# Kernel optimization log

Measured on AMD Instinct MI355X. Metric: run time of the kernel, lower is better.

Reference implementation:

```python
import jax, jax.numpy as jnp
import numpy as np

IN_F = 135; D = 512; K = 10; DCT_N = 34; IN_N = 120; OUT_N = 24
VL = K + OUT_N          # 34, window length
VN = IN_N - K - OUT_N + 1  # 87, number of windows
NSTAGE = 2
BN_SCALE = 1.0 / np.sqrt(1.0 + 1e-5)  # eval-mode BN with default running stats (mean 0, var 1)


def get_dct_matrix(N):
    dct_m = np.eye(N)
    for k in range(N):
        for i in range(N):
            w = np.sqrt(2.0 / N)
            if k == 0:
                w = np.sqrt(1.0 / N)
            dct_m[k, i] = w * np.cos(np.pi * (i + 0.5) * k / N)
    idct_m = np.linalg.inv(dct_m)
    return dct_m, idct_m

_DCT_NP, _IDCT_NP = get_dct_matrix(VL)
DCT = jnp.asarray(_DCT_NP[:DCT_N], dtype=jnp.float32)        # [34,34] (dct_n == vl)
IDCT = jnp.asarray(_IDCT_NP[:, :DCT_N], dtype=jnp.float32)   # [34,34]

WIN_IDX = np.arange(VL)[None, :] + np.arange(VN)[:, None]    # [87,34]
PAD_IDX = np.concatenate([np.arange(IN_N - K, IN_N), np.full(OUT_N, IN_N - 1)])  # last 10 frames + last frame repeated


def conv1d(x, w):
    return jax.lax.conv_general_dilated(x, w, (1,), 'VALID',
                                        dimension_numbers=('NCH', 'OIH', 'NCH'))


def gconv(x, att, w, b):
    # GraphConvolution: att @ (x @ w) + b ; x: [b,n,f_in]
    return jnp.einsum('nm,bmf->bnf', att, x @ w) + b


def bn_eval(y, g, b):
    bs, n, f = y.shape
    v = y.reshape(bs, n * f)
    v = g * (v * BN_SCALE) + b
    return v.reshape(bs, n, f)


def setup_inputs() -> dict:
    key = jax.random.key(0)
    ks = jax.random.split(key, 20)
    s = 0.05  # small init scale so tanh/att stay in sane range
    return {
        'poses':    jax.random.normal(ks[0], (256, 144, 135), jnp.float32),
        'qw1':      jax.random.normal(ks[1], (512, 135, 6)) * s,
        'qw2':      jax.random.normal(ks[2], (512, 512, 5)) * s,
        'kw1':      jax.random.normal(ks[3], (512, 135, 6)) * s,
        'kw2':      jax.random.normal(ks[4], (512, 512, 5)) * s,
        'gc1_att':  jax.random.normal(ks[5], (135, 135)) * s,
        'gc1_w':    jax.random.normal(ks[6], (68, 512)) * s,
        'gc1_b':    jax.random.normal(ks[7], (512,)) * s,
        'bn1_g':    jnp.ones((69120,), jnp.float32),
        'bn1_b':    jnp.zeros((69120,), jnp.float32),
        'gcb_att':  jax.random.normal(ks[8], (4, 135, 135)) * s,
        'gcb_w':    jax.random.normal(ks[9], (4, 512, 512)) * s,
        'gcb_b':    jax.random.normal(ks[10], (4, 512)) * s,
        'gcb_g':    jnp.ones((4, 69120), jnp.float32),
        'gcb_beta': jnp.zeros((4, 69120), jnp.float32),
        'gc7_att':  jax.random.normal(ks[11], (135, 135)) * s,
        'gc7_w':    jax.random.normal(ks[12], (512, 68)) * s,
        'gc7_b':    jax.random.normal(ks[13], (68,)) * s,
    }


def reference(poses, qw1, qw2, kw1, kw2,
              gc1_att, gc1_w, gc1_b, bn1_g, bn1_b,
              gcb_att, gcb_w, gcb_b, gcb_g, gcb_beta,
              gc7_att, gc7_w, gc7_b):
    src = poses[:, :IN_N]                      # [b,120,135]
    bs = src.shape[0]
    src_t = jnp.transpose(src, (0, 2, 1))      # [b,135,120]
    key_in = src_t[:, :, :IN_N - OUT_N] / 1000.0   # [b,135,96]
    qry_in = src_t[:, :, -K:] / 1000.0             # [b,135,10]

    key_f = jax.nn.relu(conv1d(jax.nn.relu(conv1d(key_in, kw1)), kw2))  # [b,512,87]
    qry_f = jax.nn.relu(conv1d(jax.nn.relu(conv1d(qry_in, qw1)), qw2))  # [b,512,1]

    # non-softmax attention: matmul + eps-normalize
    score = jnp.einsum('bdq,bdk->bqk', qry_f, key_f) + 1e-15   # [b,1,87]
    att = score / jnp.sum(score, axis=2, keepdims=True)

    # overlapping windows -> DCT of each window
    windows = src[:, WIN_IDX]                                   # [b,87,34,135]
    val = jnp.einsum('kt,bvtf->bvfk', DCT, windows).reshape(bs, VN, IN_F * DCT_N)
    dct_att = jnp.einsum('bqv,bvz->bqz', att, val)[:, 0].reshape(bs, IN_F, DCT_N)

    input_gcn = src[:, PAD_IDX]                                 # [b,34,135]
    dct_in = jnp.einsum('kt,btf->bfk', DCT, input_gcn)          # [b,135,34]
    x = jnp.concatenate([dct_in, dct_att], axis=-1)             # [b,135,68]

    # GCN (eval mode: dropout = identity, BN uses running stats)
    y = jnp.tanh(bn_eval(gconv(x, gc1_att, gc1_w, gc1_b), bn1_g, bn1_b))
    for i in range(NSTAGE):
        res = y
        h = jnp.tanh(bn_eval(gconv(y, gcb_att[2 * i], gcb_w[2 * i], gcb_b[2 * i]),
                             gcb_g[2 * i], gcb_beta[2 * i]))
        h = jnp.tanh(bn_eval(gconv(h, gcb_att[2 * i + 1], gcb_w[2 * i + 1], gcb_b[2 * i + 1]),
                             gcb_g[2 * i + 1], gcb_beta[2 * i + 1]))
        y = h + res
    y = gconv(y, gc7_att, gc7_w, gc7_b) + x                     # [b,135,68]

    out = jnp.einsum('tk,bfk->btf', IDCT, y[:, :, :DCT_N])      # [b,34,135]
    preds = out[:, -OUT_N:, :]                                  # [b,24,135]
    return preds
```

## Files before the change

### kernel.cpp

```cpp
#include <hip/hip_runtime.h>
#include <math.h>

#define POSE_ROWS 144
#define NF 135
#define DD 512
#define KQ 10
#define DCTN 34
#define INN 120
#define OUTN 24
#define VN 87
#define BATCH 256
#define RP 34816
#define NODEP 136
#define BSTRIDE 69632
#define BN_SCALE 0.9999950000374997f

typedef __attribute__((ext_vector_type(8))) short short8;
typedef __attribute__((ext_vector_type(4))) float floatx4;

static __device__ __forceinline__ ushort f2bf(float f) {
    unsigned u = __builtin_bit_cast(unsigned, f);
    u = (u + 0x7FFFu + ((u >> 16) & 1u)) >> 16;
    return (ushort)u;
}
static __device__ __forceinline__ float bf2f(ushort s) {
    return __builtin_bit_cast(float, (unsigned)s << 16);
}
static __device__ __forceinline__ float tanh_fast(float x) {
    float ax = __builtin_fabsf(x);
    float e = __builtin_amdgcn_exp2f(ax * -2.885390081777927f);
    float t = (1.f - e) * __builtin_amdgcn_rcpf(1.f + e);
    return __builtin_copysignf(t, x);
}
static __device__ __forceinline__ floatx4 mf(short8 a, short8 b, floatx4 c) {
    return __builtin_amdgcn_mfma_f32_16x16x32_bf16(a, b, c, 0, 0, 0);
}

#define GLOAD_LDS(gp, lp) __builtin_amdgcn_global_load_lds( \
    (const __attribute__((address_space(1))) unsigned int*)(const void*)(gp), \
    (__attribute__((address_space(3))) unsigned int*)(void*)(lp), 16, 0, 0)

#define PB_POSES 19584
#define PB_K1B   22912
#define PB_K2B   33152
#define PB_WT1   33408
#define PB_WTB   37504
#define PB_WT7   37640
#define PB_A1    37742
#define PB_AB    38147
#define PB_A7    38249
#define PB_BN    39609
#define PB_Z     39610
#define PB_DCT   39615

__global__ __launch_bounds__(256) void prep_all(
    const float* __restrict__ poses, ushort* __restrict__ pb16,
    const float* __restrict__ kw1, const float* __restrict__ qw1,
    ushort* __restrict__ Wt1k, ushort* __restrict__ Wt1q,
    const float* __restrict__ kw2, const float* __restrict__ qw2,
    ushort* __restrict__ Wt2k, ushort* __restrict__ Wt2q,
    const float* __restrict__ gc1_w, ushort* __restrict__ WT1,
    const float* __restrict__ gcb_w, ushort* __restrict__ WTb,
    const float* __restrict__ gc7_w, ushort* __restrict__ WT7,
    const float* __restrict__ gc1_att, ushort* __restrict__ A16_1,
    const float* __restrict__ gcb_att, ushort* __restrict__ A16_B,
    const float* __restrict__ gc7_att, ushort* __restrict__ A16_7,
    const float* __restrict__ bn1_g, const float* __restrict__ bn1_b,
    const float* __restrict__ gcb_g, const float* __restrict__ gcb_beta,
    const float* __restrict__ gc1_bias, const float* __restrict__ gcb_bias,
    float* __restrict__ bnT, float* __restrict__ zpadf, float* __restrict__ dct)
{
    const int blk = blockIdx.x;
    const int tid = threadIdx.x;
    if (blk < PB_POSES) {
        int idx = blk * 256 + tid;
        int i = idx % NODEP;
        int row = (idx / NODEP) % POSE_ROWS;
        int b = idx / (NODEP * POSE_ROWS);
        float v = (i < NF) ? poses[((long long)b * POSE_ROWS + row) * NF + i] * 1e-3f : 0.f;
        pb16[idx] = f2bf(v);
    } else if (blk < PB_K1B) {
        int wi = blk - PB_POSES;
        const float* src = (wi < 1664) ? kw1 : qw1;
        ushort* dst = (wi < 1664) ? Wt1k : Wt1q;
        int idx = (wi % 1664) * 256 + tid;
        int n = idx / 832, k = idx % 832;
        int h = k / 136, i = k % 136;
        float v = (i < 135 && h < 6) ? src[((long long)n * 135 + i) * 6 + h] : 0.f;
        dst[idx] = f2bf(v);
    } else if (blk < PB_K2B) {
        int wi = blk - PB_K1B;
        const float* src = (wi < 5120) ? kw2 : qw2;
        ushort* dst = (wi < 5120) ? Wt2k : Wt2q;
        int idx = (wi % 5120) * 256 + tid;
        int n = idx / 2560, k = idx % 2560;
        int h = k / 512, i = k % 512;
        dst[idx] = f2bf(src[((long long)n * 512 + i) * 5 + h]);
    } else if (blk < PB_WT1) {
        int idx = (blk - PB_K2B) * 256 + tid;
        int n = idx / 128, k = idx % 128;
        WT1[idx] = f2bf((k < 68) ? gc1_w[(long long)k * 512 + n] : 0.f);
    } else if (blk < PB_WTB) {
        int g = (blk - PB_WT1) * 256 + tid;
        int L = g >> 18, idx = g & 262143;
        int n = idx / 512, k = idx % 512;
        WTb[g] = f2bf(gcb_w[(long long)L * 262144 + (long long)k * 512 + n]);
    } else if (blk < PB_WT7) {
        int idx = (blk - PB_WTB) * 256 + tid;
        int n = idx / 512, k = idx % 512;
        WT7[idx] = f2bf(gc7_w[(long long)k * 68 + n]);
    } else if (blk < PB_A1) {
        int idx = (blk - PB_WT7) * 256 + tid;
        if (idx < 135 * 192) {
            int r = idx / 192, c = idx % 192;
            A16_1[idx] = f2bf(c < 135 ? gc1_att[r * 135 + c] : 0.f);
        }
    } else if (blk < PB_AB) {
        int idx = (blk - PB_A1) * 256 + tid;
        int r = idx / 192, c = idx % 192;
        A16_B[idx] = f2bf(c < 135 ? gcb_att[r * 135 + c] : 0.f);
    } else if (blk < PB_A7) {
        int idx = (blk - PB_AB) * 256 + tid;
        if (idx < 135 * 192) {
            int r = idx / 192, c = idx % 192;
            A16_7[idx] = f2bf(c < 135 ? gc7_att[r * 135 + c] : 0.f);
        }
    } else if (blk < PB_BN) {
        int g = (blk - PB_A7) * 256 + tid;
        int p = g / 69632, idx = g % 69632;
        int node = idx % 136, m = idx / 136;
        const float* gs = (p == 0) ? bn1_g : (gcb_g + (p - 1) * 69120);
        const float* bs = (p == 0) ? bn1_b : (gcb_beta + (p - 1) * 69120);
        const float* bp = (p == 0) ? gc1_bias : (gcb_bias + (p - 1) * 512);
        float* gt = bnT + (long long)p * 139264;
        float gg = (node < 135) ? gs[node * 512 + m] : 0.f;
        float bb = (node < 135) ? bs[node * 512 + m] : 0.f;
        float gx = gg * BN_SCALE;
        gt[idx * 2]     = gx;
        gt[idx * 2 + 1] = gx * bp[m] + bb;
    } else if (blk < PB_Z) {
        if (tid < 128) zpadf[tid] = 0.f;
    } else {
        int idx = (blk - PB_Z) * 256 + tid;
        if (idx < DCTN * DCTN) {
            int k = idx / DCTN, i = idx % DCTN;
            double w = (k == 0) ? sqrt(1.0 / DCTN) : sqrt(2.0 / DCTN);
            dct[idx] = (float)(w * cos(3.14159265358979323846 * (i + 0.5) * k / (double)DCTN));
        }
    }
}

template<int BM, int BN>
__global__ __launch_bounds__(256) void gemm2(
    const ushort* __restrict__ A, const ushort* __restrict__ Bt,
    const ushort* __restrict__ zpad,
    int M, int N, int K,
    int mode, int CNT, int Pc,
    int rpbA, long long sAw, long long sAr, long long sAbz,
    long long sBr, long long sBbz,
    float* __restrict__ C, ushort* __restrict__ C16,
    long long sCbz, long long sCm, long long sCn,
    int do_relu, const float* __restrict__ bias, int bias_mode,
    const float* __restrict__ bnTg, const float* __restrict__ bnTb,
    int do_tanh, const ushort* __restrict__ resid16, const float* __restrict__ resid32,
    int bmaj)
{
    constexpr int SM = BM / 32, SN = BN / 32;
    constexpr int RA = BM / 32, RB = BN / 32;
    __shared__ ushort As[BM * 64];
    __shared__ ushort Bs[BN * 64];

    int mb, nb;
    if (mode == 0) { mb = blockIdx.y; nb = blockIdx.x; }
    else {
        int gx = blockIdx.x;
        int x = gx & 7, s = gx >> 3;
        if (mode == 1) { mb = s % CNT; nb = x * Pc + s / CNT; }
        else           { nb = s % CNT; mb = x * Pc + s / CNT; }
    }
    const int m0 = mb * BM, n0 = nb * BN;
    if (m0 >= M || n0 >= N) return;

    const int tid = threadIdx.x;
    const int lane = tid & 63, w = tid >> 6;
    const int bz = blockIdx.z;
    const int wm = (w >> 1) * (BM / 2), wn = (w & 1) * (BN / 2);
    const int chunk = (lane & 7) ^ ((lane >> 3) & 7);

    const ushort* pA[RA]; int stA[RA];
    #pragma unroll
    for (int j = 0; j < RA; j++) {
        int m = m0 + j * 32 + w * 8 + (lane >> 3);
        bool v = m < M;
        long long off = v ? ((long long)(m / rpbA) * sAw + (long long)(m % rpbA) * sAr
                            + (long long)bz * sAbz) : 0;
        pA[j] = v ? (A + off + chunk * 8) : (zpad + chunk * 8);
        stA[j] = v ? 64 : 0;
    }
    const ushort* pB[RB]; int stB[RB];
    #pragma unroll
    for (int j = 0; j < RB; j++) {
        int n = n0 + j * 32 + w * 8 + (lane >> 3);
        bool v = n < N;
        long long off = v ? ((long long)n * sBr + (long long)bz * sBbz) : 0;
        pB[j] = v ? (Bt + off + chunk * 8) : (zpad + chunk * 8);
        stB[j] = v ? 64 : 0;
    }

    floatx4 acc[SM][SN];
    #pragma unroll
    for (int i = 0; i < SM; i++)
        #pragma unroll
        for (int j = 0; j < SN; j++)
            acc[i][j] = (floatx4){0.f, 0.f, 0.f, 0.f};

    for (int k0 = 0; k0 < K; k0 += 64) {
        #pragma unroll
        for (int j = 0; j < RA; j++)
            GLOAD_LDS(pA[j], &As[(j * 32 + w * 8) * 64]);
        #pragma unroll
        for (int j = 0; j < RB; j++)
            GLOAD_LDS(pB[j], &Bs[(j * 32 + w * 8) * 64]);
        __syncthreads();

        #pragma unroll
        for (int kk = 0; kk < 2; kk++) {
            short8 af[SM], bf[SN];
            #pragma unroll
            for (int sm = 0; sm < SM; sm++) {
                int lr = wm + sm * 16 + (lane & 15);
                int slot = ((lane >> 4) + kk * 4) ^ (lr & 7);
                af[sm] = *(const short8*)&As[lr * 64 + slot * 8];
            }
            #pragma unroll
            for (int sn = 0; sn < SN; sn++) {
                int lr = wn + sn * 16 + (lane & 15);
                int slot = ((lane >> 4) + kk * 4) ^ (lr & 7);
                bf[sn] = *(const short8*)&Bs[lr * 64 + slot * 8];
            }
            #pragma unroll
            for (int sm = 0; sm < SM; sm++)
                #pragma unroll
                for (int sn = 0; sn < SN; sn++)
                    acc[sm][sn] = mf(af[sm], bf[sn], acc[sm][sn]);
        }
        __syncthreads();

        #pragma unroll
        for (int j = 0; j < RA; j++) pA[j] += stA[j];
        #pragma unroll
        for (int j = 0; j < RB; j++) pB[j] += stB[j];
    }

    const int lc = lane & 15;
    const int lr4 = (lane >> 4) << 2;
    #pragma unroll
    for (int sm = 0; sm < SM; sm++) {
        #pragma unroll
        for (int sn = 0; sn < SN; sn++) {
            int n = n0 + wn + sn * 16 + lc;
            if (n >= N) continue;
            int node = n % 136;
            int mbv = m0 + wm + sm * 16 + lr4;
            float vv[4];
            #pragma unroll
            for (int r = 0; r < 4; r++) {
                int m = mbv + r;
                float v = acc[sm][sn][r];
                if (do_relu) v = fmaxf(v, 0.f);
                if (bias) v += (bias_mode == 1) ? bias[m < M ? m : 0] : bias[n];
                if (bnTg) {
                    long long gi = (long long)(m < M ? m : 0) * 136 + node;
                    float2 gbv = ((const float2*)bnTg)[gi];
                    v = gbv.x * v + gbv.y;
                }
                if (do_tanh) v = tanh_fast(v);
                long long addr = bmaj
                    ? (long long)(n / 136) * BSTRIDE + (long long)m * 136 + node
                    : (long long)bz * sCbz + (long long)m * sCm + (long long)n * sCn;
                if (m < M) {
                    if (resid16) v += bf2f(resid16[addr]);
                    else if (resid32) v += resid32[addr];
                    if (C) C[addr] = v;
                    if (C16 && sCm != 1) C16[addr] = f2bf(v);
                }
                vv[r] = v;
            }
            if (C16 && sCm == 1 && mbv + 3 < M) {
                ushort4 pk;
                pk.x = f2bf(vv[0]); pk.y = f2bf(vv[1]); pk.z = f2bf(vv[2]); pk.w = f2bf(vv[3]);
                *(ushort4*)&C16[(long long)bz * sCbz + mbv + (long long)n * sCn] = pk;
            }
        }
    }
}

__global__ __launch_bounds__(512) void fused_layer(
    const ushort* __restrict__ Yin,
    const ushort* __restrict__ Att,
    const ushort* __restrict__ Wt,
    const ushort* __restrict__ zpad,
    const float2* __restrict__ bnGB,
    const ushort* __restrict__ resid16,
    ushort* __restrict__ Yout)
{
    extern __shared__ ushort zs[];
    const int b = blockIdx.x;
    const int tid = threadIdx.x;
    const int lane = tid & 63, w = tid >> 6;
    const int ln = lane & 15;
    const int lk8 = (lane >> 4) * 8;
    const int lr4 = (lane >> 4) << 2;
    const long long ybase = (long long)b * BSTRIDE;
    const int cp = w * 64;

    {
        const ushort* pb[9];
        #pragma unroll
        for (int nt = 0; nt < 9; nt++) {
            int n = nt * 16 + ln;
            pb[nt] = (n < 135) ? (Att + (long long)n * 192 + lk8) : (zpad + lk8);
        }
        const ushort* pa[4];
        #pragma unroll
        for (int sm = 0; sm < 4; sm++) {
            int c = cp + sm * 16 + ln;
            pa[sm] = Yin + ybase + (long long)c * 136 + lk8;
        }
        floatx4 acc[4][9];
        #pragma unroll
        for (int i = 0; i < 4; i++)
            #pragma unroll
            for (int j = 0; j < 9; j++)
                acc[i][j] = (floatx4){0.f, 0.f, 0.f, 0.f};

        auto p1load = [&](int ks, short8 (&AF)[4]) {
            const int ko = ks * 32;
            #pragma unroll
            for (int sm = 0; sm < 4; sm++)
                AF[sm] = *(const short8*)(pa[sm] + ko);
        };
        auto p1comp = [&](int ks, short8 (&AF)[4]) {
            const int ko = ks * 32;
            short8 bf[9];
            #pragma unroll
            for (int nt = 0; nt < 9; nt++)
                bf[nt] = *(const short8*)(pb[nt] + ko);
            #pragma unroll
            for (int nt = 0; nt < 9; nt++)
                #pragma unroll
                for (int sm = 0; sm < 4; sm++)
                    acc[sm][nt] = mf(AF[sm], bf[nt], acc[sm][nt]);
        };
        short8 afA[4], afB[4];
        p1load(0, afA);
        p1load(1, afB);
        p1comp(0, afA);
        p1load(2, afA);
        p1comp(1, afB);
        p1load(3, afB);
        p1comp(2, afA);
        p1load(4, afA);
        p1comp(3, afB);
        p1comp(4, afA);

        #pragma unroll
        for (int sm = 0; sm < 4; sm++) {
            #pragma unroll
            for (int nt = 0; nt < 9; nt++) {
                int n = nt * 16 + ln;
                if (n >= 136) continue;
                int c = cp + sm * 16 + lr4;
                ushort4 pk;
                pk.x = f2bf(acc[sm][nt][0]);
                pk.y = f2bf(acc[sm][nt][1]);
                pk.z = f2bf(acc[sm][nt][2]);
                pk.w = f2bf(acc[sm][nt][3]);
                int chs = (c >> 3) ^ (n & 7);
                *(ushort4*)&zs[n * 512 + chs * 8 + (c & 7)] = pk;
            }
        }
    }
    __syncthreads();

    {
        const ushort* pw[4];
        #pragma unroll
        for (int sm = 0; sm < 4; sm++)
            pw[sm] = Wt + (long long)(cp + sm * 16 + ln) * 512 + lk8;
        int zrow[9], zx[9];
        #pragma unroll
        for (int nt = 0; nt < 9; nt++) {
            int n = nt * 16 + ln;
            int nn = (n < 136) ? n : 0;
            zrow[nt] = nn * 512;
            zx[nt] = nn & 7;
        }
        floatx4 acc[4][9];
        #pragma unroll
        for (int i = 0; i < 4; i++)
            #pragma unroll
            for (int j = 0; j < 9; j++)
                acc[i][j] = (floatx4){0.f, 0.f, 0.f, 0.f};

        auto p2load = [&](int ks, short8 (&AF)[4]) {
            const int ko = ks * 32;
            #pragma unroll
            for (int sm = 0; sm < 4; sm++)
                AF[sm] = *(const short8*)(pw[sm] + ko);
        };
        auto p2comp = [&](int ks, short8 (&AF)[4]) {
            const int kchunk = ks * 4 + (lane >> 4);
            short8 bf[9];
            #pragma unroll
            for (int nt = 0; nt < 9; nt++)
                bf[nt] = *(const short8*)&zs[zrow[nt] + (kchunk ^ zx[nt]) * 8];
            #pragma unroll
            for (int nt = 0; nt < 9; nt++)
                #pragma unroll
                for (int sm = 0; sm < 4; sm++)
                    acc[sm][nt] = mf(AF[sm], bf[nt], acc[sm][nt]);
        };
        short8 afA[4], afB[4];
        p2load(0, afA);
        p2load(1, afB);
        #pragma unroll
        for (int kp = 0; kp < 7; kp++) {
            p2comp(2 * kp, afA);
            p2load(2 * kp + 2, afA);
            p2comp(2 * kp + 1, afB);
            p2load(2 * kp + 3, afB);
        }
        p2comp(14, afA);
        p2comp(15, afB);

        #pragma unroll
        for (int nt = 0; nt < 9; nt++) {
            int n = nt * 16 + ln;
            int nn = (n < 136) ? n : 0;
            float2 gb[16];
            ushort rr[16];
            #pragma unroll
            for (int sm = 0; sm < 4; sm++)
                #pragma unroll
                for (int r = 0; r < 4; r++) {
                    int m = cp + sm * 16 + lr4 + r;
                    gb[sm * 4 + r] = bnGB[(long long)m * 136 + nn];
                    rr[sm * 4 + r] = resid16 ? resid16[ybase + (long long)m * 136 + nn]
                                             : (ushort)0;
                }
            if (n >= 136) continue;
            #pragma unroll
            for (int sm = 0; sm < 4; sm++)
                #pragma unroll
                for (int r = 0; r < 4; r++) {
                    int m = cp + sm * 16 + lr4 + r;
                    float v = acc[sm][nt][r];
                    v = gb[sm * 4 + r].x * v + gb[sm * 4 + r].y;
                    v = tanh_fast(v);
                    if (resid16) v += bf2f(rr[sm * 4 + r]);
                    Yout[ybase + (long long)m * 136 + n] = f2bf(v);
                }
        }
    }
}

__global__ __launch_bounds__(256) void att_k(const float* __restrict__ kf, const float* __restrict__ qf,
                                             float* __restrict__ att) {
    int b = blockIdx.x;
    int tid = threadIdx.x;
    int lane = tid & 63, w = tid >> 6;
    __shared__ float s[96];
    __shared__ float ssum;
    const float* qb = qf + b * DD + lane * 8;
    float4 q0 = *(const float4*)qb;
    float4 q1 = *(const float4*)(qb + 4);
    const float* kb = kf + (long long)b * VN * DD;
    for (int v = w; v < VN; v += 4) {
        const float* kr = kb + v * DD + lane * 8;
        float4 k0 = *(const float4*)kr;
        float4 k1 = *(const float4*)(kr + 4);
        float p = q0.x * k0.x + q0.y * k0.y + q0.z * k0.z + q0.w * k0.w
                + q1.x * k1.x + q1.y * k1.y + q1.z * k1.z + q1.w * k1.w;
        #pragma unroll
        for (int off = 32; off; off >>= 1) p += __shfl_xor(p, off);
        if (lane == 0) s[v] = p + 1e-15f;
    }
    __syncthreads();
    if (tid < 64) {
        float p2 = (tid < VN ? s[tid] : 0.f) + ((tid + 64) < VN ? s[tid + 64] : 0.f);
        #pragma unroll
        for (int off = 32; off; off >>= 1) p2 += __shfl_xor(p2, off);
        if (tid == 0) ssum = p2;
    }
    __syncthreads();
    float inv = 1.f / ssum;
    for (int v = tid; v < VN; v += 256) att[b * VN + v] = s[v] * inv;
}

__global__ void weighted_k(const float* __restrict__ poses, const float* __restrict__ att,
                           float* __restrict__ w34) {
    int t = blockIdx.x;
    int b = blockIdx.y;
    int f = threadIdx.x;
    if (f >= NF) return;
    const float* pb = poses + (long long)b * POSE_ROWS * NF + t * NF + f;
    const float* ab = att + b * VN;
    float acc = 0.f;
    for (int v = 0; v < VN; v++) acc += ab[v] * pb[v * NF];
    w34[(long long)b * DCTN * NF + t * NF + f] = acc;
}

__global__ void build_x(const float* __restrict__ poses, const float* __restrict__ w34,
                        const float* __restrict__ dctm, float* __restrict__ x32,
                        ushort* __restrict__ xT16) {
    int idx = blockIdx.x * 256 + threadIdx.x;
    if (idx >= BATCH * NF * 68) return;
    int kk = idx % 68;
    int f = (idx / 68) % NF;
    int b = idx / (68 * NF);
    float acc = 0.f;
    if (kk < DCTN) {
        const float* pb = poses + (long long)b * POSE_ROWS * NF;
        #pragma unroll
        for (int t = 0; t < DCTN; t++) {
            int row = (t < KQ) ? (INN - KQ + t) : (INN - 1);
            acc += dctm[kk * DCTN + t] * pb[row * NF + f];
        }
    } else {
        int k2 = kk - DCTN;
        const float* wb = w34 + (long long)b * DCTN * NF + f;
        #pragma unroll
        for (int t = 0; t < DCTN; t++) acc += dctm[k2 * DCTN + t] * wb[t * NF];
    }
    long long R = (long long)b * NODEP + f;
    x32[R * 68 + kk] = acc;
    xT16[(long long)kk * RP + R] = f2bf(acc);
}

__global__ void idct_out(const float* __restrict__ h32, const float* __restrict__ dctm,
                         float* __restrict__ out) {
    int idx = blockIdx.x * 256 + threadIdx.x;
    if (idx >= BATCH * OUTN * NF) return;
    int f = idx % NF;
    int t = (idx / NF) % OUTN;
    int b = idx / (NF * OUTN);
    const float* yr = h32 + ((long long)b * NODEP + f) * 68;
    float acc = 0.f;
    #pragma unroll
    for (int k = 0; k < DCTN; k++) acc += dctm[k * DCTN + (KQ + t)] * yr[k];
    out[idx] = acc;
}

extern "C" void kernel_launch(void* const* d_in, const int* in_sizes, int n_in,
                              void* d_out, int out_size, void* d_ws, size_t ws_size,
                              hipStream_t stream) {
    const float* poses   = (const float*)d_in[0];
    const float* qw1     = (const float*)d_in[1];
    const float* qw2     = (const float*)d_in[2];
    const float* kw1     = (const float*)d_in[3];
    const float* kw2     = (const float*)d_in[4];
    const float* gc1_att = (const float*)d_in[5];
    const float* gc1_w   = (const float*)d_in[6];
    const float* gc1_b   = (const float*)d_in[7];
    const float* bn1_g   = (const float*)d_in[8];
    const float* bn1_b   = (const float*)d_in[9];
    const float* gcb_att = (const float*)d_in[10];
    const float* gcb_w   = (const float*)d_in[11];
    const float* gcb_b   = (const float*)d_in[12];
    const float* gcb_g   = (const float*)d_in[13];
    const float* gcb_beta= (const float*)d_in[14];
    const float* gc7_att = (const float*)d_in[15];
    const float* gc7_w   = (const float*)d_in[16];
    const float* gc7_b   = (const float*)d_in[17];
    float* out = (float*)d_out;
    float* w = (float*)d_ws;

    float* dct   = w;
    float* att   = w + 1280;
    float* w34   = w + 23808;
    float* x32   = w + 1198848;
    float* h32   = w + 3566336;
    float* qf    = w + 5933824;
    ushort* su   = (ushort*)(w + 6064896);
    ushort* WT1    = su;
    ushort* WTb    = su + 65536;
    ushort* WT7    = su + 1114112;
    ushort* A16_1  = su + 1148928;
    ushort* A16_B  = su + 1174848;
    ushort* A16_7  = su + 1278528;
    float* bnT   = w + 6717120;
    float* kf    = w + 7413440;
    ushort* R2   = (ushort*)(w + 18816704);
    ushort* yT16  = R2;
    ushort* r1k16 = R2;
    ushort* r1q16 = R2 + 11927552;
    ushort* R3   = (ushort*)(w + 27729600);
    ushort* hT16  = R3;
    ushort* pb16  = R3;
    ushort* Wt1k  = R3 + 5013504;
    ushort* Wt1q  = R3 + 5439488;
    ushort* Wt2k  = R3 + 5865472;
    ushort* Wt2q  = R3 + 7176192;
    ushort* R4   = (ushort*)(w + 36642496);
    ushort* zN16  = R4;
    ushort* xT16  = R4;
    ushort* z116  = R4 + 2367488;
    float* zpadf = w + 45555392;
    const ushort* zpad = (const ushort*)zpadf;

    const int INF_RPB = 1 << 30;

    static int lds_set = 0;
    if (!lds_set) {
        hipFuncSetAttribute((const void*)fused_layer,
                            hipFuncAttributeMaxDynamicSharedMemorySize, 139264);
        lds_set = 1;
    }

    prep_all<<<PB_DCT, 256, 0, stream>>>(
        poses, pb16, kw1, qw1, Wt1k, Wt1q, kw2, qw2, Wt2k, Wt2q,
        gc1_w, WT1, gcb_w, WTb, gc7_w, WT7,
        gc1_att, A16_1, gcb_att, A16_B, gc7_att, A16_7,
        bn1_g, bn1_b, gcb_g, gcb_beta, gc1_b, gcb_b, bnT, zpadf, dct);

    gemm2<128,64><<<dim3(1472, 1, 1), 256, 0, stream>>>(pb16, Wt1k, zpad, 23296, 512, 832,
        2, 8, 23, 91, 19584LL, 136LL, 0LL, 832LL, 0LL,
        (float*)nullptr, r1k16, 0LL, 512LL, 1LL, 1, nullptr, 0, nullptr, nullptr, 0, nullptr, nullptr, 0);
    gemm2<128,128><<<dim3(4, 10, 1), 256, 0, stream>>>(pb16 + 110*136, Wt1q, zpad, 1280, 512, 832,
        0, 0, 0, 5, 19584LL, 136LL, 0LL, 832LL, 0LL,
        (float*)nullptr, r1q16, 0LL, 512LL, 1LL, 1, nullptr, 0, nullptr, nullptr, 0, nullptr, nullptr, 0);
    gemm2<128,64><<<dim3(1408, 1, 1), 256, 0, stream>>>(r1k16, Wt2k, zpad, 22272, 512, 2560,
        2, 8, 22, 87, 46592LL, 512LL, 0LL, 2560LL, 0LL,
        kf, (ushort*)nullptr, 0LL, 512LL, 1LL, 1, nullptr, 0, nullptr, nullptr, 0, nullptr, nullptr, 0);
    gemm2<64,64><<<dim3(8, 4, 1), 256, 0, stream>>>(r1q16, Wt2q, zpad, 256, 512, 2560,
        0, 0, 0, INF_RPB, 0LL, 2560LL, 0LL, 2560LL, 0LL,
        qf, (ushort*)nullptr, 0LL, 512LL, 1LL, 1, nullptr, 0, nullptr, nullptr, 0, nullptr, nullptr, 0);

    att_k<<<BATCH, 256, 0, stream>>>(kf, qf, att);
    weighted_k<<<dim3(DCTN, BATCH), 192, 0, stream>>>(poses, att, w34);
    build_x<<<(BATCH * NF * 68 + 255) / 256, 256, 0, stream>>>(poses, w34, dct, x32, xT16);

    gemm2<64,64><<<dim3(3, 2, BATCH), 256, 0, stream>>>(xT16, A16_1, zpad, 68, 135, 192,
        0, 0, 0, INF_RPB, 0LL, (long long)RP, 136LL, 192LL, 0LL,
        (float*)nullptr, z116, 10880LL, 1LL, 80LL, 0, nullptr, 0, nullptr, nullptr, 0, nullptr, nullptr, 0);
    gemm2<128,64><<<dim3(2176, 1, 1), 256, 0, stream>>>(WT1, z116, zpad, 512, RP, 128,
        1, 4, 68, INF_RPB, 0LL, 128LL, 0LL, 80LL, 0LL,
        (float*)nullptr, yT16, 0LL, (long long)RP, 1LL, 0, nullptr, 0, bnT, nullptr, 1, nullptr, nullptr, 1);

    for (int L = 0; L < 4; L++) {
        const ushort* min = (L & 1) ? hT16 : yT16;
        ushort* mout = (L & 1) ? yT16 : hT16;
        fused_layer<<<dim3(BATCH, 1, 1), 512, 139264, stream>>>(
            min, A16_B + L * 25920, WTb + L * 262144, zpad,
            (const float2*)(bnT + (1 + L) * 139264),
            (L & 1) ? yT16 : (const ushort*)nullptr, mout);
    }

    gemm2<64,64><<<dim3(3, 8, BATCH), 256, 0, stream>>>(yT16, A16_7, zpad, 512, 135, 192,
        0, 0, 0, INF_RPB, 0LL, 136LL, (long long)BSTRIDE, 192LL, 0LL,
        (float*)nullptr, zN16, 69632LL, 1LL, 512LL, 0, nullptr, 0, nullptr, nullptr, 0, nullptr, nullptr, 0);
    gemm2<64,64><<<dim3(1088, 1, 1), 256, 0, stream>>>(zN16, WT7, zpad, RP, 68, 512,
        2, 2, 68, INF_RPB, 0LL, 512LL, 0LL, 512LL, 0LL,
        h32, (ushort*)nullptr, 0LL, 68LL, 1LL, 0, gc7_b, 2, nullptr, nullptr, 0, nullptr, x32, 0);

    idct_out<<<(BATCH * OUTN * NF + 255) / 256, 256, 0, stream>>>(h32, dct, out);
}
```

Baseline: 823.6 us.

## Split fused GCN layer across two blocks per batch along node dimension

The fused graph-conv layer kernel now launches two blocks per batch element, each handling half of the 136 node columns (68 each). This halves per-block shared memory and accumulator registers and doubles the grid from 256 to 512 blocks, filling more compute units on the 256-CU device. The trade-off is that each half recomputes nothing extra but pads 68 nodes up to 80 (5 tiles of 16), so some MFMA work is wasted, and the weight matrix is streamed twice per batch.

```diff
diff --git a/kernel.cpp b/kernel.cpp
--- a/kernel.cpp
+++ b/kernel.cpp
@@ -305,7 +305,9 @@
     ushort* __restrict__ Yout)
 {
     extern __shared__ ushort zs[];
-    const int b = blockIdx.x;
+    const int b  = blockIdx.x >> 1;
+    const int nh = blockIdx.x & 1;
+    const int nbase = nh * 68;
     const int tid = threadIdx.x;
     const int lane = tid & 63, w = tid >> 6;
     const int ln = lane & 15;
@@ -315,11 +317,13 @@
     const int cp = w * 64;
 
     {
-        const ushort* pb[9];
-        #pragma unroll
-        for (int nt = 0; nt < 9; nt++) {
-            int n = nt * 16 + ln;
-            pb[nt] = (n < 135) ? (Att + (long long)n * 192 + lk8) : (zpad + lk8);
+        const ushort* pb[5];
+        #pragma unroll
+        for (int nt = 0; nt < 5; nt++) {
+            int local = nt * 16 + ln;
+            int ng = nbase + local;
+            pb[nt] = (local < 68 && ng < 135) ? (Att + (long long)ng * 192 + lk8)
+                                              : (zpad + lk8);
         }
         const ushort* pa[4];
         #pragma unroll
@@ -327,11 +331,11 @@
             int c = cp + sm * 16 + ln;
             pa[sm] = Yin + ybase + (long long)c * 136 + lk8;
         }
-        floatx4 acc[4][9];
+        floatx4 acc[4][5];
         #pragma unroll
         for (int i = 0; i < 4; i++)
             #pragma unroll
-            for (int j = 0; j < 9; j++)
+            for (int j = 0; j < 5; j++)
                 acc[i][j] = (floatx4){0.f, 0.f, 0.f, 0.f};
 
         auto p1load = [&](int ks, short8 (&AF)[4]) {
@@ -342,12 +346,12 @@
         };
         auto p1comp = [&](int ks, short8 (&AF)[4]) {
             const int ko = ks * 32;
-            short8 bf[9];
-            #pragma unroll
-            for (int nt = 0; nt < 9; nt++)
+            short8 bf[5];
+            #pragma unroll
+            for (int nt = 0; nt < 5; nt++)
                 bf[nt] = *(const short8*)(pb[nt] + ko);
             #pragma unroll
-            for (int nt = 0; nt < 9; nt++)
+            for (int nt = 0; nt < 5; nt++)
                 #pragma unroll
                 for (int sm = 0; sm < 4; sm++)
                     acc[sm][nt] = mf(AF[sm], bf[nt], acc[sm][nt]);
@@ -367,17 +371,17 @@
         #pragma unroll
         for (int sm = 0; sm < 4; sm++) {
             #pragma unroll
-            for (int nt = 0; nt < 9; nt++) {
-                int n = nt * 16 + ln;
-                if (n >= 136) continue;
+            for (int nt = 0; nt < 5; nt++) {
+                int local = nt * 16 + ln;
+                if (local >= 68) continue;
                 int c = cp + sm * 16 + lr4;
                 ushort4 pk;
                 pk.x = f2bf(acc[sm][nt][0]);
                 pk.y = f2bf(acc[sm][nt][1]);
                 pk.z = f2bf(acc[sm][nt][2]);
                 pk.w = f2bf(acc[sm][nt][3]);
-                int chs = (c >> 3) ^ (n & 7);
-                *(ushort4*)&zs[n * 512 + chs * 8 + (c & 7)] = pk;
+                int chs = (c >> 3) ^ (local & 7);
+                *(ushort4*)&zs[local * 512 + chs * 8 + (c & 7)] = pk;
             }
         }
     }
@@ -388,19 +392,19 @@
         #pragma unroll
         for (int sm = 0; sm < 4; sm++)
             pw[sm] = Wt + (long long)(cp + sm * 16 + ln) * 512 + lk8;
-        int zrow[9], zx[9];
-        #pragma unroll
-        for (int nt = 0; nt < 9; nt++) {
-            int n = nt * 16 + ln;
-            int nn = (n < 136) ? n : 0;
-            zrow[nt] = nn * 512;
-            zx[nt] = nn & 7;
-        }
-        floatx4 acc[4][9];
+        int zrow[5], zx[5];
+        #pragma unroll
+        for (int nt = 0; nt < 5; nt++) {
+            int local = nt * 16 + ln;
+            int ll = (local < 68) ? local : 0;
+            zrow[nt] = ll * 512;
+            zx[nt] = ll & 7;
+        }
+        floatx4 acc[4][5];
         #pragma unroll
         for (int i = 0; i < 4; i++)
             #pragma unroll
-            for (int j = 0; j < 9; j++)
+            for (int j = 0; j < 5; j++)
                 acc[i][j] = (floatx4){0.f, 0.f, 0.f, 0.f};
 
         auto p2load = [&](int ks, short8 (&AF)[4]) {
@@ -411,12 +415,12 @@
         };
         auto p2comp = [&](int ks, short8 (&AF)[4]) {
             const int kchunk = ks * 4 + (lane >> 4);
-            short8 bf[9];
-            #pragma unroll
-            for (int nt = 0; nt < 9; nt++)
+            short8 bf[5];
+            #pragma unroll
+            for (int nt = 0; nt < 5; nt++)
                 bf[nt] = *(const short8*)&zs[zrow[nt] + (kchunk ^ zx[nt]) * 8];
             #pragma unroll
-            for (int nt = 0; nt < 9; nt++)
+            for (int nt = 0; nt < 5; nt++)
                 #pragma unroll
                 for (int sm = 0; sm < 4; sm++)
                     acc[sm][nt] = mf(AF[sm], bf[nt], acc[sm][nt]);
@@ -435,9 +439,10 @@
         p2comp(15, afB);
 
         #pragma unroll
-        for (int nt = 0; nt < 9; nt++) {
-            int n = nt * 16 + ln;
-            int nn = (n < 136) ? n : 0;
+        for (int nt = 0; nt < 5; nt++) {
+            int local = nt * 16 + ln;
+            int ll = (local < 68) ? local : 0;
+            int n = nbase + ll;
             float2 gb[16];
             ushort rr[16];
             #pragma unroll
@@ -445,11 +450,11 @@
                 #pragma unroll
                 for (int r = 0; r < 4; r++) {
                     int m = cp + sm * 16 + lr4 + r;
-                    gb[sm * 4 + r] = bnGB[(long long)m * 136 + nn];
-                    rr[sm * 4 + r] = resid16 ? resid16[ybase + (long long)m * 136 + nn]
+                    gb[sm * 4 + r] = bnGB[(long long)m * 136 + n];
+                    rr[sm * 4 + r] = resid16 ? resid16[ybase + (long long)m * 136 + n]
                                              : (ushort)0;
                 }
-            if (n >= 136) continue;
+            if (local >= 68) continue;
             #pragma unroll
             for (int sm = 0; sm < 4; sm++)
                 #pragma unroll
@@ -614,7 +619,7 @@
     static int lds_set = 0;
     if (!lds_set) {
         hipFuncSetAttribute((const void*)fused_layer,
-                            hipFuncAttributeMaxDynamicSharedMemorySize, 139264);
+                            hipFuncAttributeMaxDynamicSharedMemorySize, 69632);
         lds_set = 1;
     }
 
@@ -651,7 +656,7 @@
     for (int L = 0; L < 4; L++) {
         const ushort* min = (L & 1) ? hT16 : yT16;
         ushort* mout = (L & 1) ? yT16 : hT16;
-        fused_layer<<<dim3(BATCH, 1, 1), 512, 139264, stream>>>(
+        fused_layer<<<dim3(2 * BATCH, 1, 1), 512, 69632, stream>>>(
             min, A16_B + L * 25920, WTb + L * 262144, zpad,
             (const float2*)(bnT + (1 + L) * 139264),
             (L & 1) ? yT16 : (const ushort*)nullptr, mout);
```

Result: slower. 1.026 ms (+24.6%).
